# Optimization experiments

Hardware: AMD Instinct MI355X
Metric: run time of the kernel (lower is better)

Reference implementation:

```python
import jax, jax.numpy as jnp
import numpy as np

D_MODEL = 2048
D_INNER = 4096
D_XB = 1024
D_STATE = 64
HEADDIM = 64
NHEADS = D_INNER // HEADDIM      # 64
NXB = D_XB // HEADDIM
D_CONV = 4
CHUNK = 128
EPS = 1e-5
D_FF = 8192
CONV_DIM = D_XB + D_XB + D_INNER             # conv over [x, B, C]
D_IN_PROJ = D_INNER + D_XB + D_XB + D_INNER + NHEADS  # z, x, B, C, dt


def setup_inputs() -> dict:
    key = jax.random.key(0)
    ks = jax.random.split(key, 8)
    s = 0.02
    return {
        "hidden_states": jax.random.normal(ks[0], (2, 2048, D_MODEL), jnp.float32),
        "in_proj_w": jax.random.normal(ks[1], (D_MODEL, D_IN_PROJ), jnp.float32) * s,
        "conv_w": jax.random.normal(ks[2], (CONV_DIM, D_CONV), jnp.float32) * 0.1,
        "conv_b": jnp.zeros((CONV_DIM,), jnp.float32),
        "dt_bias": jnp.log(jnp.expm1(jnp.linspace(0.001, 0.1, NHEADS, dtype=jnp.float32))),
        "A_log": jnp.log(jnp.linspace(1.0, 16.0, NHEADS, dtype=jnp.float32)),
        "D": jnp.ones((NHEADS,), jnp.float32),
        "norm_w": jnp.ones((D_INNER,), jnp.float32),
        "out_proj_w": jax.random.normal(ks[3], (D_INNER, D_MODEL), jnp.float32) * s,
        "ln1_w": jnp.ones((D_MODEL,), jnp.float32),
        "ln2_w": jnp.ones((D_MODEL,), jnp.float32),
        "gate_w": jax.random.normal(ks[4], (D_MODEL, D_FF), jnp.float32) * s,
        "up_w": jax.random.normal(ks[5], (D_MODEL, D_FF), jnp.float32) * s,
        "down_w": jax.random.normal(ks[6], (D_FF, D_MODEL), jnp.float32) * s,
    }


def rmsnorm(x, w, eps=EPS):
    return x * jax.lax.rsqrt(jnp.mean(x * x, axis=-1, keepdims=True) + eps) * w


def causal_depthwise_conv(x, w, b):
    # x: [b, l, c], w: [c, k] depthwise causal conv
    k = w.shape[1]
    xp = jnp.pad(x, ((0, 0), (k - 1, 0), (0, 0)))
    out = jax.lax.conv_general_dilated(
        xp.transpose(0, 2, 1), w[:, None, :], (1,), "VALID",
        feature_group_count=x.shape[-1])
    return out.transpose(0, 2, 1) + b


def ssd_chunked(xdt, dA, Bm, Cm):
    # Mamba2 SSD chunked scan. xdt: [b,l,h,p] (x*dt), dA: [b,l,h] (dt*A), Bm/Cm: [b,l,h,n]
    b, l, h, p = xdt.shape
    n = Bm.shape[-1]
    c, q = l // CHUNK, CHUNK
    xdt = xdt.reshape(b, c, q, h, p)
    Bm = Bm.reshape(b, c, q, h, n)
    Cm = Cm.reshape(b, c, q, h, n)
    dA = dA.reshape(b, c, q, h).transpose(0, 3, 1, 2)   # [b,h,c,q]
    dAc = jnp.cumsum(dA, axis=-1)                        # [b,h,c,q]
    # intra-chunk (diagonal blocks)
    seg = dAc[..., :, None] - dAc[..., None, :]          # [b,h,c,q,q]
    mask = jnp.tril(jnp.ones((q, q), bool))
    Lm = jnp.where(mask, jnp.exp(seg), 0.0)
    Y_diag = jnp.einsum("bcqhn,bcshn,bhcqs,bcshp->bcqhp", Cm, Bm, Lm, xdt)
    # per-chunk final states
    decay_states = jnp.exp(dAc[..., -1:] - dAc)          # [b,h,c,q]
    states = jnp.einsum("bcqhn,bhcq,bcqhp->bchpn", Bm, decay_states, xdt)
    chunk_decay = jnp.exp(dAc[..., -1])                  # [b,h,c]
    def step(carry, inp):
        s, d = inp
        new = s + d[:, :, None, None] * carry
        return new, carry
    init = jnp.zeros((b, h, p, n), xdt.dtype)
    _, prevs = jax.lax.scan(step, init,
                            (states.transpose(1, 0, 2, 3, 4),
                             chunk_decay.transpose(2, 0, 1)))
    # prevs: [c,b,h,p,n] = state entering each chunk; inter-chunk contribution
    Y_off = jnp.einsum("bcqhn,cbhpn,bhcq->bcqhp", Cm, prevs, jnp.exp(dAc))
    return (Y_diag + Y_off).reshape(b, l, h, p)


def mamba2(x, in_proj_w, conv_w, conv_b, dt_bias, A_log, Dp, norm_w, out_proj_w):
    b, l, _ = x.shape
    zxbcdt = x @ in_proj_w
    z, xb, Bc, Cc, dt = jnp.split(
        zxbcdt, [D_INNER, D_INNER + D_XB, D_INNER + 2 * D_XB, 2 * D_INNER + 2 * D_XB], axis=-1)
    xBC = jax.nn.silu(causal_depthwise_conv(jnp.concatenate([xb, Bc, Cc], -1), conv_w, conv_b))
    xb, Bc, Cc = jnp.split(xBC, [D_XB, 2 * D_XB], axis=-1)
    dt = jax.nn.softplus(dt + dt_bias)                   # [b,l,h]
    A = -jnp.exp(A_log)                                  # [h]
    rep = NHEADS // NXB
    x_h = jnp.repeat(xb.reshape(b, l, NXB, HEADDIM), rep, axis=2)   # [b,l,h,p]
    B_h = jnp.repeat(Bc.reshape(b, l, NXB, D_STATE), rep, axis=2)   # [b,l,h,n]
    C_h = Cc.reshape(b, l, NHEADS, D_STATE)
    y = ssd_chunked(x_h * dt[..., None], dt * A, B_h, C_h)
    y = y + Dp[None, None, :, None] * x_h
    y = y.reshape(b, l, D_INNER)
    y = rmsnorm(y * jax.nn.silu(z), norm_w)
    return y @ out_proj_w


def reference(hidden_states, in_proj_w, conv_w, conv_b, dt_bias, A_log, D,
              norm_w, out_proj_w, ln1_w, ln2_w, gate_w, up_w, down_w):
    residual = hidden_states
    h = rmsnorm(hidden_states, ln1_w)
    h = residual + mamba2(h, in_proj_w, conv_w, conv_b, dt_bias, A_log, D, norm_w, out_proj_w)
    residual = h
    h2 = rmsnorm(h, ln2_w)
    mlp = (jax.nn.silu(h2 @ gate_w) * (h2 @ up_w)) @ down_w
    return residual + mlp
```

## Files before the change

kernel.cpp:

```cpp
#include <hip/hip_runtime.h>
#include <hip/hip_bf16.h>
#include <stdint.h>

#define TOK     4096
#define LSEQ    2048
#define DMODEL  2048
#define DINNER  4096
#define DXB     1024
#define DIP     10304
#define NPROJ   10240
#define CONVDIM 6144
#define DFF     8192
#define NH      64
#define CHUNK   128
#define NCHUNK  16
#define EPSF    1e-5f

typedef __hip_bfloat16 bf16_t;
typedef __bf16 bf16x8 __attribute__((ext_vector_type(8)));
typedef unsigned short u16x8 __attribute__((ext_vector_type(8)));
typedef float f32x4 __attribute__((ext_vector_type(4)));

__device__ __forceinline__ float siluf(float x) { return x / (1.f + __expf(-x)); }
__device__ __forceinline__ float bf2f(bf16_t h) { return __bfloat162float(h); }
__device__ __forceinline__ float bits2f(unsigned short u) { return __uint_as_float((unsigned)u << 16); }
__device__ __forceinline__ unsigned short f2bits(float f) {
  union { bf16_t h; unsigned short u; } cv; cv.h = __float2bfloat16(f); return cv.u;
}
__device__ __forceinline__ void gload_lds16(const void* g, void* l) {
  __builtin_amdgcn_global_load_lds((const __attribute__((address_space(1))) void*)g,
                                   (__attribute__((address_space(3))) void*)l, 16, 0, 0);
}

__global__ void k_tcvt(const float* __restrict__ in, bf16_t* __restrict__ out,
                       int R, int C, int rs, int r_off, int c_off) {
  __shared__ float tile[32][33];
  int c0 = blockIdx.x * 32, r0 = blockIdx.y * 32;
  int tx = threadIdx.x, ty = threadIdx.y;
  for (int i = 0; i < 32; i += 8)
    tile[ty + i][tx] = in[(size_t)(r_off + r0 + ty + i) * rs + c_off + c0 + tx];
  __syncthreads();
  for (int i = 0; i < 32; i += 8)
    out[(size_t)(c0 + ty + i) * R + r0 + tx] = __float2bfloat16(tile[tx][ty + i]);
}

__global__ __launch_bounds__(256) void k_rmsnorm_bf16(const float* __restrict__ x,
                                                      const float* __restrict__ w,
                                                      bf16_t* __restrict__ out, int D) {
  int row = blockIdx.x, tid = threadIdx.x;
  const float* xr = x + (size_t)row * D;
  float ss = 0.f;
  for (int j = tid; j < D; j += 256) { float v = xr[j]; ss += v * v; }
  __shared__ float sbuf[4];
  for (int o = 32; o > 0; o >>= 1) ss += __shfl_down(ss, o, 64);
  if ((tid & 63) == 0) sbuf[tid >> 6] = ss;
  __syncthreads();
  float rinv = rsqrtf((sbuf[0] + sbuf[1] + sbuf[2] + sbuf[3]) / D + EPSF);
  bf16_t* orow = out + (size_t)row * D;
  for (int j = tid; j < D; j += 256) orow[j] = __float2bfloat16(xr[j] * rinv * w[j]);
}

__global__ __launch_bounds__(256) void k_gemm(const bf16_t* __restrict__ A,
                                              const bf16_t* __restrict__ Bt,
                                              const float* auxf,
                                              void* outp, void* out2,
                                              int M, int N, int K, int mode) {
  __shared__ unsigned short As[128][32];
  __shared__ unsigned short Bs[128][32];
  const int tid = threadIdx.x;
  const int n0 = blockIdx.x * 128, m0 = blockIdx.y * 128;
  const int lane = tid & 63, w = tid >> 6;
  const int wm = (w >> 1) * 64, wn = (w & 1) * 64;
  const int l16 = lane & 15, quad = lane >> 4;

  const int srow = lane >> 2;
  const int scol = (lane & 3) * 8;
  const unsigned short* Ag = (const unsigned short*)A + (size_t)(m0 + w * 32 + srow) * K + scol;
  const unsigned short* Bg = (const unsigned short*)Bt + (size_t)(n0 + w * 32 + srow) * K + scol;
  const size_t K16 = (size_t)16 * K;
  unsigned short* lA0 = &As[w * 32][0];
  unsigned short* lA1 = &As[w * 32 + 16][0];
  unsigned short* lB0 = &Bs[w * 32][0];
  unsigned short* lB1 = &Bs[w * 32 + 16][0];

  f32x4 acc[4][4] = {};
  for (int k0 = 0; k0 < K; k0 += 32) {
    __syncthreads();
    gload_lds16(Ag, lA0); gload_lds16(Ag + K16, lA1);
    gload_lds16(Bg, lB0); gload_lds16(Bg + K16, lB1);
    Ag += 32; Bg += 32;
    __syncthreads();
    bf16x8 af[4], bfv[4];
#pragma unroll
    for (int mi = 0; mi < 4; mi++) af[mi] = *(const bf16x8*)&As[wm + mi * 16 + l16][quad * 8];
#pragma unroll
    for (int ni = 0; ni < 4; ni++) bfv[ni] = *(const bf16x8*)&Bs[wn + ni * 16 + l16][quad * 8];
#pragma unroll
    for (int mi = 0; mi < 4; mi++)
#pragma unroll
      for (int ni = 0; ni < 4; ni++)
        acc[mi][ni] = __builtin_amdgcn_mfma_f32_16x16x32_bf16(af[mi], bfv[ni], acc[mi][ni], 0, 0, 0);
  }
#pragma unroll
  for (int mi = 0; mi < 4; mi++) {
    const int gm = m0 + wm + mi * 16 + quad * 4;
#pragma unroll
    for (int ni = 0; ni < 4; ni++) {
      const int gn = n0 + wn + ni * 16 + l16;
#pragma unroll
      for (int r = 0; r < 4; r++) {
        const size_t idx = (size_t)(gm + r) * N + gn;
        float v = acc[mi][ni][r];
        if (mode == 0) {
          ((float*)outp)[idx] = v + (auxf ? auxf[idx] : 0.f);
        } else if (mode == 1) {
          ((bf16_t*)outp)[idx] = __float2bfloat16(siluf(v));
        } else if (mode == 2) {
          bf16_t* o = (bf16_t*)outp;
          o[idx] = __float2bfloat16(v * bf2f(o[idx]));
        } else {
          if (gn < DINNER)
            ((bf16_t*)outp)[(size_t)(gm + r) * DINNER + gn] = __float2bfloat16(v);
          else
            ((bf16_t*)out2)[(size_t)(gm + r) * CONVDIM + (gn - DINNER)] = __float2bfloat16(v);
        }
      }
    }
  }
}

__global__ __launch_bounds__(256) void k_conv(const bf16_t* __restrict__ xr,
                                              const float* __restrict__ cw,
                                              const float* __restrict__ cb,
                                              bf16_t* __restrict__ xBC) {
  const int row = blockIdx.x;
  const int t = row & (LSEQ - 1);
  const float4* wv = (const float4*)cw;
  const float4* bv = (const float4*)cb;
  for (int c4 = threadIdx.x; c4 < CONVDIM / 4; c4 += 256) {
    const int c = c4 * 4;
    float4 w0 = wv[c], w1 = wv[c + 1], w2 = wv[c + 2], w3 = wv[c + 3];
    float4 bb = bv[c4];
    const bf16_t* base = xr + (size_t)row * CONVDIM + c;
    ushort4 u0 = *(const ushort4*)base;
    ushort4 u1 = {0,0,0,0}, u2 = {0,0,0,0}, u3 = {0,0,0,0};
    if (t >= 1) u1 = *(const ushort4*)(base - CONVDIM);
    if (t >= 2) u2 = *(const ushort4*)(base - 2 * CONVDIM);
    if (t >= 3) u3 = *(const ushort4*)(base - 3 * CONVDIM);
    ushort4 o;
    o.x = f2bits(siluf(bb.x + w0.x*bits2f(u3.x) + w0.y*bits2f(u2.x) + w0.z*bits2f(u1.x) + w0.w*bits2f(u0.x)));
    o.y = f2bits(siluf(bb.y + w1.x*bits2f(u3.y) + w1.y*bits2f(u2.y) + w1.z*bits2f(u1.y) + w1.w*bits2f(u0.y)));
    o.z = f2bits(siluf(bb.z + w2.x*bits2f(u3.z) + w2.y*bits2f(u2.z) + w2.z*bits2f(u1.z) + w2.w*bits2f(u0.z)));
    o.w = f2bits(siluf(bb.w + w3.x*bits2f(u3.w) + w3.y*bits2f(u2.w) + w3.z*bits2f(u1.w) + w3.w*bits2f(u0.w)));
    *(ushort4*)&xBC[(size_t)row * CONVDIM + c] = o;
  }
}

__global__ __launch_bounds__(256) void k_dt(const float* __restrict__ hs,
                                            const float* __restrict__ ln1,
                                            const float* __restrict__ Wip,
                                            const float* __restrict__ dt_bias,
                                            float* __restrict__ dt) {
  const int row = blockIdx.x, tid = threadIdx.x;
  __shared__ float xs[DMODEL];
  __shared__ float red[4][64];
  __shared__ float sbuf[4];
  const float* xr = hs + (size_t)row * DMODEL;
  float ss = 0.f;
  for (int j = tid; j < DMODEL; j += 256) { float v = xr[j]; ss += v * v; }
  for (int o = 32; o > 0; o >>= 1) ss += __shfl_down(ss, o, 64);
  if ((tid & 63) == 0) sbuf[tid >> 6] = ss;
  __syncthreads();
  float rinv = rsqrtf((sbuf[0] + sbuf[1] + sbuf[2] + sbuf[3]) / DMODEL + EPSF);
  for (int j = tid; j < DMODEL; j += 256) xs[j] = xr[j] * rinv * ln1[j];
  __syncthreads();
  const int h = tid & 63, kq = tid >> 6;
  float acc = 0.f;
  for (int k = kq * 512; k < (kq + 1) * 512; k++)
    acc += xs[k] * Wip[(size_t)k * DIP + 2 * DINNER + 2 * DXB + h];
  red[kq][h] = acc;
  __syncthreads();
  if (tid < 64) {
    float v = red[0][tid] + red[1][tid] + red[2][tid] + red[3][tid] + dt_bias[tid];
    float sp = (v > 20.f) ? v : log1pf(__expf(v));
    dt[(size_t)row * NH + tid] = sp;
  }
}

__global__ void k_dacum(const float* __restrict__ dt, const float* __restrict__ A_log,
                        float* __restrict__ dAc, float* __restrict__ cdec) {
  const int bh = blockIdx.x;
  const int b = bh >> 6, h = bh & 63;
  const int q = threadIdx.x;
  const float Ah = -__expf(A_log[h]);
  __shared__ float s[CHUNK];
  for (int c = 0; c < NCHUNK; c++) {
    int row = b * LSEQ + c * CHUNK + q;
    float v = dt[(size_t)row * NH + h] * Ah;
    s[q] = v;
    __syncthreads();
    for (int off = 1; off < CHUNK; off <<= 1) {
      float tadd = (q >= off) ? s[q - off] : 0.f;
      __syncthreads();
      s[q] += tadd;
      __syncthreads();
    }
    float r = s[q];
    dAc[((size_t)bh * NCHUNK + c) * CHUNK + q] = r;
    if (q == CHUNK - 1) cdec[bh * NCHUNK + c] = __expf(r);
    __syncthreads();
  }
}

__global__ __launch_bounds__(256) void k_states(const bf16_t* __restrict__ xBC,
                                                const float* __restrict__ dtp,
                                                const float* __restrict__ dAc,
                                                float* __restrict__ states) {
  const int blk = blockIdx.x;
  const int h = blk & 63, c = (blk >> 6) & 15, b = blk >> 10;
  const int tid = threadIdx.x;
  const int n0 = (tid >> 4) * 4, p0 = (tid & 15) * 4;
  const int rowb = b * LSEQ + c * CHUNK;
  const int boff = DXB + (h >> 2) * 64, xoff = (h >> 2) * 64;
  __shared__ float Bq[64][64];
  __shared__ float xq[64][64];
  __shared__ float dac_s[CHUNK];
  if (tid < CHUNK) dac_s[tid] = dAc[((size_t)(b * 64 + h) * NCHUNK + c) * CHUNK + tid];
  __syncthreads();
  const float last = dac_s[CHUNK - 1];
  f32x4 acc[4] = {};
  for (int half = 0; half < 2; half++) {
    __syncthreads();
    for (int idx = tid; idx < 64 * 64; idx += 256) {
      int q = idx >> 6, col = idx & 63;
      int row = rowb + half * 64 + q;
      float dec = __expf(last - dac_s[half * 64 + q]);
      const bf16_t* src = xBC + (size_t)row * CONVDIM;
      Bq[q][col] = bf2f(src[boff + col]) * dec;
      xq[q][col] = bf2f(src[xoff + col]) * dtp[(size_t)row * NH + h];
    }
    __syncthreads();
    for (int q = 0; q < 64; q++) {
      f32x4 bv = *(const f32x4*)&Bq[q][n0];
      f32x4 xv = *(const f32x4*)&xq[q][p0];
#pragma unroll
      for (int r = 0; r < 4; r++) acc[r] += bv[r] * xv;
    }
  }
  float* sb = states + (size_t)blk * 4096;
#pragma unroll
  for (int r = 0; r < 4; r++) *(f32x4*)&sb[(n0 + r) * 64 + p0] = acc[r];
}

__global__ __launch_bounds__(256) void k_scan(const float* __restrict__ states,
                                              const float* __restrict__ cdec,
                                              float* __restrict__ prevs) {
  const int gid = blockIdx.x * 256 + threadIdx.x;
  const int e = gid & 4095;
  const int h = (gid >> 12) & 63;
  const int b = gid >> 18;
  float carry = 0.f;
  for (int c = 0; c < NCHUNK; c++) {
    size_t idx = ((size_t)((b * 16 + c) * 64 + h)) * 4096 + e;
    prevs[idx] = carry;
    carry = states[idx] + cdec[(b * 64 + h) * NCHUNK + c] * carry;
  }
}

__global__ __launch_bounds__(256) void k_yout(const bf16_t* __restrict__ xBC,
                                              const float* __restrict__ dtp,
                                              const float* __restrict__ dAc,
                                              const float* __restrict__ prevs,
                                              const float* __restrict__ Dp,
                                              bf16_t* __restrict__ y) {
  const int blk = blockIdx.x;
  const int h = blk & 63, c = (blk >> 6) & 15, b = blk >> 10;
  const int tid = threadIdx.x;
  const int lane = tid & 63, w = tid >> 6;
  const int l16 = lane & 15, quad = lane >> 4;
  const int rowb = b * LSEQ + c * CHUNK;
  const int xoff = (h >> 2) * 64, boff = DXB + (h >> 2) * 64, coff = 2 * DXB + h * 64;

  __shared__ __align__(16) unsigned short CtX[128 * 72];
  __shared__ __align__(16) unsigned short BtP[128 * 136];
  __shared__ __align__(16) unsigned short pvT[64 * 72];
  __shared__ float dac_s[CHUNK];
  __shared__ float dt_s[CHUNK];

  if (tid < CHUNK) {
    dac_s[tid] = dAc[((size_t)(b * 64 + h) * NCHUNK + c) * CHUNK + tid];
    dt_s[tid] = dtp[(size_t)(rowb + tid) * NH + h];
  }
  for (int idx = tid; idx < 1024; idx += 256) {
    const int i = idx >> 3, e0 = (idx & 7) * 8;
    const unsigned short* src = (const unsigned short*)xBC + (size_t)(rowb + i) * CONVDIM;
    *(u16x8*)&CtX[i * 72 + e0] = *(const u16x8*)&src[coff + e0];
    *(u16x8*)&BtP[i * 136 + e0] = *(const u16x8*)&src[boff + e0];
  }
  {
    const float* pvsrc = prevs + (size_t)blk * 4096;
    for (int idx = tid; idx < 1024; idx += 256) {
      const int n = idx >> 4, p0 = (idx & 15) * 4;
      f32x4 v = *(const f32x4*)&pvsrc[n * 64 + p0];
#pragma unroll
      for (int r = 0; r < 4; r++) pvT[(p0 + r) * 72 + n] = f2bits(v[r]);
    }
  }
  __syncthreads();

  const int wm = (w >> 1) * 64, wn = (w & 1) * 64;
  f32x4 acc1[4][4] = {};
  if (wm >= wn) {
#pragma unroll
    for (int kk = 0; kk < 2; kk++) {
      bf16x8 af[4], bv[4];
#pragma unroll
      for (int mi = 0; mi < 4; mi++)
        af[mi] = *(const bf16x8*)&CtX[(wm + mi * 16 + l16) * 72 + kk * 32 + quad * 8];
#pragma unroll
      for (int ni = 0; ni < 4; ni++)
        bv[ni] = *(const bf16x8*)&BtP[(wn + ni * 16 + l16) * 136 + kk * 32 + quad * 8];
#pragma unroll
      for (int mi = 0; mi < 4; mi++)
#pragma unroll
        for (int ni = 0; ni < 4; ni++)
          acc1[mi][ni] = __builtin_amdgcn_mfma_f32_16x16x32_bf16(af[mi], bv[ni], acc1[mi][ni], 0, 0, 0);
    }
  }
  __syncthreads();

#pragma unroll
  for (int mi = 0; mi < 4; mi++) {
#pragma unroll
    for (int r = 0; r < 4; r++) {
      const int i = wm + mi * 16 + quad * 4 + r;
      const float di = dac_s[i];
#pragma unroll
      for (int ni = 0; ni < 4; ni++) {
        const int j = wn + ni * 16 + l16;
        const float v = (j <= i) ? __expf(di - dac_s[j]) * acc1[mi][ni][r] : 0.f;
        BtP[i * 136 + j] = f2bits(v);
      }
    }
  }
  for (int idx = tid; idx < 1024; idx += 256) {
    const int i = idx >> 3, e0 = (idx & 7) * 8;
    const float sc = __expf(dac_s[i]);
    u16x8 v = *(u16x8*)&CtX[i * 72 + e0];
#pragma unroll
    for (int r = 0; r < 8; r++) v[r] = f2bits(bits2f(v[r]) * sc);
    *(u16x8*)&CtX[i * 72 + e0] = v;
  }
  __syncthreads();

  const int wm2 = w * 32;
  f32x4 acc2[2][4] = {};
#pragma unroll
  for (int kk = 0; kk < 2; kk++) {
    bf16x8 af[2], bv[4];
#pragma unroll
    for (int mi = 0; mi < 2; mi++)
      af[mi] = *(const bf16x8*)&CtX[(wm2 + mi * 16 + l16) * 72 + kk * 32 + quad * 8];
#pragma unroll
    for (int ni = 0; ni < 4; ni++)
      bv[ni] = *(const bf16x8*)&pvT[(ni * 16 + l16) * 72 + kk * 32 + quad * 8];
#pragma unroll
    for (int mi = 0; mi < 2; mi++)
#pragma unroll
      for (int ni = 0; ni < 4; ni++)
        acc2[mi][ni] = __builtin_amdgcn_mfma_f32_16x16x32_bf16(af[mi], bv[ni], acc2[mi][ni], 0, 0, 0);
  }
  __syncthreads();

  for (int idx = tid; idx < 1024; idx += 256) {
    const int j = idx >> 3, p0 = (idx & 7) * 8;
    u16x8 v = *(const u16x8*)((const unsigned short*)xBC + (size_t)(rowb + j) * CONVDIM + xoff + p0);
    const float dtj = dt_s[j];
#pragma unroll
    for (int r = 0; r < 8; r++) CtX[(p0 + r) * 136 + j] = f2bits(bits2f(v[r]) * dtj);
  }
  __syncthreads();

#pragma unroll
  for (int kk = 0; kk < 4; kk++) {
    bf16x8 af[2], bv[4];
#pragma unroll
    for (int mi = 0; mi < 2; mi++)
      af[mi] = *(const bf16x8*)&BtP[(wm2 + mi * 16 + l16) * 136 + kk * 32 + quad * 8];
#pragma unroll
    for (int ni = 0; ni < 4; ni++)
      bv[ni] = *(const bf16x8*)&CtX[(ni * 16 + l16) * 136 + kk * 32 + quad * 8];
#pragma unroll
    for (int mi = 0; mi < 2; mi++)
#pragma unroll
      for (int ni = 0; ni < 4; ni++)
        acc2[mi][ni] = __builtin_amdgcn_mfma_f32_16x16x32_bf16(af[mi], bv[ni], acc2[mi][ni], 0, 0, 0);
  }

  const float Dh = Dp[h];
#pragma unroll
  for (int mi = 0; mi < 2; mi++) {
#pragma unroll
    for (int r = 0; r < 4; r++) {
      const int i = wm2 + mi * 16 + quad * 4 + r;
      const float df = Dh / dt_s[i];
      bf16_t* orow = y + (size_t)(rowb + i) * DINNER + h * 64;
#pragma unroll
      for (int ni = 0; ni < 4; ni++) {
        const int p = ni * 16 + l16;
        const float v = acc2[mi][ni][r] + df * bits2f(CtX[p * 136 + i]);
        orow[p] = __float2bfloat16(v);
      }
    }
  }
}

__global__ __launch_bounds__(256) void k_gatenorm(const bf16_t* __restrict__ y,
                                                  const bf16_t* __restrict__ z,
                                                  const float* __restrict__ nw,
                                                  bf16_t* __restrict__ outp) {
  const int row = blockIdx.x, tid = threadIdx.x;
  const bf16_t* yr = y + (size_t)row * DINNER;
  const bf16_t* zr = z + (size_t)row * DINNER;
  float vals[16];
  float ss = 0.f;
#pragma unroll
  for (int k = 0; k < 16; k++) {
    int j = tid + k * 256;
    float v = bf2f(yr[j]) * siluf(bf2f(zr[j]));
    vals[k] = v; ss += v * v;
  }
  __shared__ float sbuf[4];
  for (int o = 32; o > 0; o >>= 1) ss += __shfl_down(ss, o, 64);
  if ((tid & 63) == 0) sbuf[tid >> 6] = ss;
  __syncthreads();
  float rinv = rsqrtf((sbuf[0] + sbuf[1] + sbuf[2] + sbuf[3]) / DINNER + EPSF);
  bf16_t* orow = outp + (size_t)row * DINNER;
#pragma unroll
  for (int k = 0; k < 16; k++) {
    int j = tid + k * 256;
    orow[j] = __float2bfloat16(vals[k] * rinv * nw[j]);
  }
}

__global__ void k_diag(float* out, float mb) { out[0] = mb; }

static constexpr size_t OFF_WBUF = 0;
static constexpr size_t SZ_WBUF  = (size_t)NPROJ * DMODEL * 2;
static constexpr size_t OFF_Z    = OFF_WBUF + SZ_WBUF;
static constexpr size_t SZ_Z     = (size_t)TOK * DINNER * 2;
static constexpr size_t OFF_XBC  = OFF_Z + SZ_Z;
static constexpr size_t SZ_XBC   = (size_t)TOK * CONVDIM * 2;
static constexpr size_t OFF_DT   = OFF_XBC + SZ_XBC;
static constexpr size_t SZ_DT    = (size_t)TOK * NH * 4;
static constexpr size_t OFF_DAC  = OFF_DT + SZ_DT;
static constexpr size_t SZ_DAC   = (size_t)TOK * NH * 4;
static constexpr size_t OFF_CDEC = OFF_DAC + SZ_DAC;
static constexpr size_t SZ_CDEC  = (size_t)2 * 64 * NCHUNK * 4;
static constexpr size_t OFF_G    = OFF_CDEC + ((SZ_CDEC + 4095) & ~(size_t)4095);
static constexpr size_t SZ_G     = (size_t)2 * NCHUNK * 64 * 4096 * 4;
static constexpr size_t OFF_H    = OFF_G + SZ_G;
static constexpr size_t SZ_H     = (size_t)TOK * CONVDIM * 2;
static constexpr size_t OFF_I    = OFF_H + SZ_H;
static constexpr size_t SZ_I     = (size_t)2 * NCHUNK * 64 * 4096 * 4;
static constexpr size_t WS_NEED  = OFF_I + SZ_I;

extern "C" void kernel_launch(void* const* d_in, const int* in_sizes, int n_in,
                              void* d_out, int out_size, void* d_ws, size_t ws_size,
                              hipStream_t stream) {
  (void)in_sizes; (void)n_in; (void)out_size;
  if (ws_size < WS_NEED) {
    k_diag<<<1, 1, 0, stream>>>((float*)d_out, (float)(ws_size / 1048576.0));
    return;
  }

  const float* hidden     = (const float*)d_in[0];
  const float* in_proj_w  = (const float*)d_in[1];
  const float* conv_w     = (const float*)d_in[2];
  const float* conv_b     = (const float*)d_in[3];
  const float* dt_bias    = (const float*)d_in[4];
  const float* A_log      = (const float*)d_in[5];
  const float* Dv         = (const float*)d_in[6];
  const float* norm_w     = (const float*)d_in[7];
  const float* out_proj_w = (const float*)d_in[8];
  const float* ln1_w      = (const float*)d_in[9];
  const float* ln2_w      = (const float*)d_in[10];
  const float* gate_w     = (const float*)d_in[11];
  const float* up_w       = (const float*)d_in[12];
  const float* down_w     = (const float*)d_in[13];

  char* ws = (char*)d_ws;
  bf16_t* Wbuf  = (bf16_t*)(ws + OFF_WBUF);
  bf16_t* z     = (bf16_t*)(ws + OFF_Z);
  bf16_t* xBC   = (bf16_t*)(ws + OFF_XBC);
  float*  hbuf  = (float*)(ws + OFF_XBC);
  float*  dtb   = (float*)(ws + OFF_DT);
  float*  dAc   = (float*)(ws + OFF_DAC);
  float*  cdec  = (float*)(ws + OFF_CDEC);
  float*  prevs = (float*)(ws + OFF_G);
  bf16_t* h2n   = (bf16_t*)(ws + OFF_G);
  bf16_t* xbcr  = (bf16_t*)(ws + OFF_H);
  bf16_t* yn    = (bf16_t*)(ws + OFF_H);
  bf16_t* act   = (bf16_t*)(ws + OFF_H);
  bf16_t* xn1   = (bf16_t*)(ws + OFF_I);
  float*  states= (float*)(ws + OFF_I);
  bf16_t* y     = (bf16_t*)(ws + OFF_I);

  dim3 tb(32, 8);

  k_tcvt<<<dim3(NPROJ / 32, DMODEL / 32), tb, 0, stream>>>(in_proj_w, Wbuf, DMODEL, NPROJ, DIP, 0, 0);
  k_rmsnorm_bf16<<<TOK, 256, 0, stream>>>(hidden, ln1_w, xn1, DMODEL);
  k_gemm<<<dim3(NPROJ / 128, TOK / 128), 256, 0, stream>>>(xn1, Wbuf, nullptr, z, xbcr, TOK, NPROJ, DMODEL, 3);
  k_conv<<<TOK, 256, 0, stream>>>(xbcr, conv_w, conv_b, xBC);
  k_dt<<<TOK, 256, 0, stream>>>(hidden, ln1_w, in_proj_w, dt_bias, dtb);
  k_dacum<<<128, 128, 0, stream>>>(dtb, A_log, dAc, cdec);
  k_states<<<2048, 256, 0, stream>>>(xBC, dtb, dAc, states);
  k_scan<<<2048, 256, 0, stream>>>(states, cdec, prevs);
  k_yout<<<2048, 256, 0, stream>>>(xBC, dtb, dAc, prevs, Dv, y);
  k_gatenorm<<<TOK, 256, 0, stream>>>(y, z, norm_w, yn);
  k_tcvt<<<dim3(DMODEL / 32, DINNER / 32), tb, 0, stream>>>(out_proj_w, Wbuf, DINNER, DMODEL, DMODEL, 0, 0);
  k_gemm<<<dim3(DMODEL / 128, TOK / 128), 256, 0, stream>>>(yn, Wbuf, hidden, hbuf, nullptr, TOK, DMODEL, DINNER, 0);

  k_rmsnorm_bf16<<<TOK, 256, 0, stream>>>(hbuf, ln2_w, h2n, DMODEL);
  for (int g = 0; g < 2; g++) {
    const int HF = DFF / 2;
    k_tcvt<<<dim3(HF / 32, DMODEL / 32), tb, 0, stream>>>(gate_w, Wbuf, DMODEL, HF, DFF, 0, g * HF);
    k_gemm<<<dim3(HF / 128, TOK / 128), 256, 0, stream>>>(h2n, Wbuf, nullptr, act, nullptr, TOK, HF, DMODEL, 1);
    k_tcvt<<<dim3(HF / 32, DMODEL / 32), tb, 0, stream>>>(up_w, Wbuf, DMODEL, HF, DFF, 0, g * HF);
    k_gemm<<<dim3(HF / 128, TOK / 128), 256, 0, stream>>>(h2n, Wbuf, nullptr, act, nullptr, TOK, HF, DMODEL, 2);
    k_tcvt<<<dim3(DMODEL / 32, HF / 32), tb, 0, stream>>>(down_w, Wbuf, HF, DMODEL, DMODEL, g * HF, 0);
    k_gemm<<<dim3(DMODEL / 128, TOK / 128), 256, 0, stream>>>(act, Wbuf, g == 0 ? hbuf : (float*)d_out,
                                                              d_out, nullptr, TOK, DMODEL, HF, 0);
  }
}
```

Before: 1.807 ms.

## Add 256x256-tile double-buffered GEMM for in_proj, gate and up projections

Adds a new GEMM kernel with 256x256 output tiles, 512 threads, and direct global-to-LDS loads into XOR-swizzled, double-buffered shared memory. It uses explicit waitcnt/barrier pipelining and raises wave priority around the MFMA block. The kernel is used for the in_proj and the gate/up MLP GEMMs to increase operand reuse per loaded tile and overlap loads with compute. The trade-off is higher register and LDS use per block and fewer blocks, which may hurt occupancy or tail balance (e.g. in_proj gets 40x16 blocks).

```diff
diff --git a/kernel.cpp b/kernel.cpp
--- a/kernel.cpp
+++ b/kernel.cpp
@@ -111,6 +111,108 @@
       for (int r = 0; r < 4; r++) {
         const size_t idx = (size_t)(gm + r) * N + gn;
         float v = acc[mi][ni][r];
+        if (mode == 0) {
+          ((float*)outp)[idx] = v + (auxf ? auxf[idx] : 0.f);
+        } else if (mode == 1) {
+          ((bf16_t*)outp)[idx] = __float2bfloat16(siluf(v));
+        } else if (mode == 2) {
+          bf16_t* o = (bf16_t*)outp;
+          o[idx] = __float2bfloat16(v * bf2f(o[idx]));
+        } else {
+          if (gn < DINNER)
+            ((bf16_t*)outp)[(size_t)(gm + r) * DINNER + gn] = __float2bfloat16(v);
+          else
+            ((bf16_t*)out2)[(size_t)(gm + r) * CONVDIM + (gn - DINNER)] = __float2bfloat16(v);
+        }
+      }
+    }
+  }
+}
+
+__global__ __launch_bounds__(512) void k_gemm256(const bf16_t* __restrict__ A,
+                                                 const bf16_t* __restrict__ Bt,
+                                                 const float* auxf,
+                                                 void* outp, void* out2,
+                                                 int M, int N, int K, int mode) {
+  __shared__ __align__(16) unsigned short lds[2][2][16384];
+  const int tid = threadIdx.x;
+  const int lane = tid & 63, w = tid >> 6;
+  const int wm = w >> 2, wn = w & 3;
+  const int l16 = lane & 15, quad = lane >> 4;
+  const int n0 = blockIdx.x * 256, m0 = blockIdx.y * 256;
+
+  const int srow = lane >> 3;
+  const int sslot = (lane & 7) ^ srow;
+  const unsigned short* Ag = (const unsigned short*)A + (size_t)(m0 + w * 8 + srow) * K + sslot * 8;
+  const unsigned short* Bg = (const unsigned short*)Bt + (size_t)(n0 + w * 8 + srow) * K + sslot * 8;
+  const size_t rowadv = (size_t)64 * K;
+
+  f32x4 acc[8][4] = {};
+  const int NT = K >> 6;
+
+#define STAGE256(buf, coloff)                                            \
+  do {                                                                   \
+    unsigned short* la_ = &lds[buf][0][w * 512];                         \
+    unsigned short* lb_ = &lds[buf][1][w * 512];                         \
+    _Pragma("unroll")                                                    \
+    for (int c_ = 0; c_ < 4; c_++) {                                     \
+      gload_lds16(Ag + (coloff) + c_ * rowadv, la_ + c_ * 4096);         \
+      gload_lds16(Bg + (coloff) + c_ * rowadv, lb_ + c_ * 4096);         \
+    }                                                                    \
+  } while (0)
+
+  STAGE256(0, 0);
+  STAGE256(1, 64);
+
+  for (int t = 0; t < NT; t++) {
+    const int cur = t & 1;
+    if (t < NT - 1) asm volatile("s_waitcnt vmcnt(8)" ::: "memory");
+    else            asm volatile("s_waitcnt vmcnt(0)" ::: "memory");
+    __builtin_amdgcn_s_barrier();
+    bf16x8 af[2][8], bv[2][4];
+    const unsigned short* la = &lds[cur][0][0];
+    const unsigned short* lb = &lds[cur][1][0];
+#pragma unroll
+    for (int kk = 0; kk < 2; kk++) {
+#pragma unroll
+      for (int f = 0; f < 8; f++) {
+        const int row = wm * 128 + f * 16 + l16;
+        const int slot = (kk * 4 + quad) ^ (row & 7);
+        af[kk][f] = *(const bf16x8*)&la[row * 64 + slot * 8];
+      }
+#pragma unroll
+      for (int n = 0; n < 4; n++) {
+        const int row = wn * 64 + n * 16 + l16;
+        const int slot = (kk * 4 + quad) ^ (row & 7);
+        bv[kk][n] = *(const bf16x8*)&lb[row * 64 + slot * 8];
+      }
+    }
+    asm volatile("s_waitcnt lgkmcnt(0)" ::: "memory");
+    __builtin_amdgcn_sched_barrier(0);
+    __builtin_amdgcn_s_barrier();
+    if (t + 2 < NT) STAGE256(cur, (size_t)(t + 2) * 64);
+    __builtin_amdgcn_s_setprio(1);
+#pragma unroll
+    for (int kk = 0; kk < 2; kk++)
+#pragma unroll
+      for (int f = 0; f < 8; f++)
+#pragma unroll
+        for (int n = 0; n < 4; n++)
+          acc[f][n] = __builtin_amdgcn_mfma_f32_16x16x32_bf16(af[kk][f], bv[kk][n], acc[f][n], 0, 0, 0);
+    __builtin_amdgcn_s_setprio(0);
+  }
+#undef STAGE256
+
+#pragma unroll
+  for (int f = 0; f < 8; f++) {
+    const int gm = m0 + wm * 128 + f * 16 + quad * 4;
+#pragma unroll
+    for (int n = 0; n < 4; n++) {
+      const int gn = n0 + wn * 64 + n * 16 + l16;
+#pragma unroll
+      for (int r = 0; r < 4; r++) {
+        const size_t idx = (size_t)(gm + r) * N + gn;
+        float v = acc[f][n][r];
         if (mode == 0) {
           ((float*)outp)[idx] = v + (auxf ? auxf[idx] : 0.f);
         } else if (mode == 1) {
@@ -510,7 +612,7 @@
 
   k_tcvt<<<dim3(NPROJ / 32, DMODEL / 32), tb, 0, stream>>>(in_proj_w, Wbuf, DMODEL, NPROJ, DIP, 0, 0);
   k_rmsnorm_bf16<<<TOK, 256, 0, stream>>>(hidden, ln1_w, xn1, DMODEL);
-  k_gemm<<<dim3(NPROJ / 128, TOK / 128), 256, 0, stream>>>(xn1, Wbuf, nullptr, z, xbcr, TOK, NPROJ, DMODEL, 3);
+  k_gemm256<<<dim3(NPROJ / 256, TOK / 256), 512, 0, stream>>>(xn1, Wbuf, nullptr, z, xbcr, TOK, NPROJ, DMODEL, 3);
   k_conv<<<TOK, 256, 0, stream>>>(xbcr, conv_w, conv_b, xBC);
   k_dt<<<TOK, 256, 0, stream>>>(hidden, ln1_w, in_proj_w, dt_bias, dtb);
   k_dacum<<<128, 128, 0, stream>>>(dtb, A_log, dAc, cdec);
@@ -525,9 +627,9 @@
   for (int g = 0; g < 2; g++) {
     const int HF = DFF / 2;
     k_tcvt<<<dim3(HF / 32, DMODEL / 32), tb, 0, stream>>>(gate_w, Wbuf, DMODEL, HF, DFF, 0, g * HF);
-    k_gemm<<<dim3(HF / 128, TOK / 128), 256, 0, stream>>>(h2n, Wbuf, nullptr, act, nullptr, TOK, HF, DMODEL, 1);
+    k_gemm256<<<dim3(HF / 256, TOK / 256), 512, 0, stream>>>(h2n, Wbuf, nullptr, act, nullptr, TOK, HF, DMODEL, 1);
     k_tcvt<<<dim3(HF / 32, DMODEL / 32), tb, 0, stream>>>(up_w, Wbuf, DMODEL, HF, DFF, 0, g * HF);
-    k_gemm<<<dim3(HF / 128, TOK / 128), 256, 0, stream>>>(h2n, Wbuf, nullptr, act, nullptr, TOK, HF, DMODEL, 2);
+    k_gemm256<<<dim3(HF / 256, TOK / 256), 512, 0, stream>>>(h2n, Wbuf, nullptr, act, nullptr, TOK, HF, DMODEL, 2);
     k_tcvt<<<dim3(DMODEL / 32, HF / 32), tb, 0, stream>>>(down_w, Wbuf, HF, DMODEL, DMODEL, g * HF, 0);
     k_gemm<<<dim3(DMODEL / 128, TOK / 128), 256, 0, stream>>>(act, Wbuf, g == 0 ? hbuf : (float*)d_out,
                                                               d_out, nullptr, TOK, DMODEL, HF, 0);
```

Measured after the change: 1.619 ms. -10.4%, faster.
